# Optimization experiments

Hardware: AMD Instinct MI355X
Metric: run time of the kernel (lower is better)

Reference implementation:

```python
import jax, jax.numpy as jnp
import numpy as np

B, U, I, H = 1024, 8, 512, 512


def setup_inputs() -> dict:
    key = jax.random.key(0)
    ks = jax.random.split(key, 6)
    s_i = 1.0 / np.sqrt(H)  # torch GRU init: U(-1/sqrt(H), 1/sqrt(H))
    inputs = jax.random.normal(ks[0], (B, U, I), dtype=jnp.float32)
    hidden = jax.random.normal(ks[1], (B, U, H), dtype=jnp.float32)
    W_ih = jax.random.uniform(ks[2], (U, 3 * H, I), minval=-s_i, maxval=s_i, dtype=jnp.float32)
    W_hh = jax.random.uniform(ks[3], (U, 3 * H, H), minval=-s_i, maxval=s_i, dtype=jnp.float32)
    b_ih = jax.random.uniform(ks[4], (U, 3 * H), minval=-s_i, maxval=s_i, dtype=jnp.float32)
    b_hh = jax.random.uniform(ks[5], (U, 3 * H), minval=-s_i, maxval=s_i, dtype=jnp.float32)
    return {"inputs": inputs, "hidden": hidden, "W_ih": W_ih, "W_hh": W_hh, "b_ih": b_ih, "b_hh": b_hh}


def reference(inputs, hidden, W_ih, W_hh, b_ih, b_hh):
    # Grouped single-step GRU: all num_units cells computed in one batched matmul pair.
    # gx, gh: [B, U, 3H]
    gx = jnp.einsum('bui,ugi->bug', inputs, W_ih) + b_ih[None]
    gh = jnp.einsum('buh,ugh->bug', hidden, W_hh) + b_hh[None]
    xr, xz, xn = jnp.split(gx, 3, axis=-1)
    hr, hz, hn = jnp.split(gh, 3, axis=-1)
    r = jax.nn.sigmoid(xr + hr)
    z = jax.nn.sigmoid(xz + hz)
    n = jnp.tanh(xn + r * hn)
    return (1.0 - z) * n + z * hidden
```

## Files before the change

### kernel.cpp

```cpp
#include <hip/hip_runtime.h>
#include <hip/hip_bf16.h>
#include <stdint.h>


#define B_ 1024
#define U_ 8
#define I_ 512
#define H_ 512
#define KDIM 512

#define NX (B_ * U_ * I_)
#define NW (U_ * 3 * H_ * I_)
#define OFF_X 0
#define OFF_H NX
#define OFF_WIH (2 * NX)
#define OFF_WHH (2 * NX + NW)
#define NTOT (2 * NX + 2 * NW)
#define WS_NEED ((size_t)NTOT * 2)

#define BM 64
#define BN 64
#define BK 64
#define ESTR 68

typedef __attribute__((ext_vector_type(8))) short short8;
typedef __attribute__((ext_vector_type(4))) float floatx4;

__device__ __forceinline__ unsigned int pk2bf(float a, float b) {
    float2 f2; f2.x = a; f2.y = b;
    union { __hip_bfloat162 h; unsigned int u; } cv;
    cv.h = __float22bfloat162_rn(f2);
    return cv.u;
}

__device__ __forceinline__ void async16(const void* g, void* l) {
    __builtin_amdgcn_global_load_lds(
        (const __attribute__((address_space(1))) void*)g,
        (__attribute__((address_space(3))) void*)l, 16, 0, 0);
}

__global__ __launch_bounds__(256)
void convert_bf16_kernel(const float* __restrict__ x, const float* __restrict__ h,
                         const float* __restrict__ wih, const float* __restrict__ whh,
                         unsigned short* __restrict__ ws)
{
    const size_t base = ((size_t)blockIdx.x * 256 + threadIdx.x) * 8;
    const float* src; size_t off;
    if (base < (size_t)OFF_H)        { src = x;   off = OFF_X; }
    else if (base < (size_t)OFF_WIH) { src = h;   off = OFF_H; }
    else if (base < (size_t)OFF_WHH) { src = wih; off = OFF_WIH; }
    else                             { src = whh; off = OFF_WHH; }
    const float4 v0 = *(const float4*)(src + (base - off));
    const float4 v1 = *(const float4*)(src + (base - off) + 4);
    uint4 o;
    o.x = pk2bf(v0.x, v0.y);
    o.y = pk2bf(v0.z, v0.w);
    o.z = pk2bf(v1.x, v1.y);
    o.w = pk2bf(v1.z, v1.w);
    *(uint4*)(ws + base) = o;
}

union Smem {
    unsigned short bf[8][64 * 64];
    float ep[3][BM * ESTR];
};

__global__ __launch_bounds__(512, 4)
void gru_main_kernel(const unsigned short* __restrict__ ws,
                     const float* __restrict__ hidden,
                     const float* __restrict__ b_ih,
                     const float* __restrict__ b_hh,
                     float* __restrict__ out)
{
    const int u  = blockIdx.x >> 3;
    const int nb = blockIdx.x & 7;
    const int mb = blockIdx.y;
    const int b0 = mb * BM;
    const int h0 = nb * BN;

    const int tid  = threadIdx.x;
    const int lane = tid & 63;
    const int wave = tid >> 6;
    const int lr   = lane & 15;
    const int q    = lane >> 4;
    const int wm   = wave & 1;
    const int wn   = (wave >> 1) & 1;
    const int g2   = wave >> 2;

    __shared__ Smem smem;

    const unsigned short* gbase; int grstr;
    if (wave == 0)      { gbase = ws + OFF_X + ((size_t)b0 * U_ + u) * I_; grstr = U_ * I_; }
    else if (wave == 1) { gbase = ws + OFF_H + ((size_t)b0 * U_ + u) * H_; grstr = U_ * H_; }
    else if (wave <= 4) { int g = wave - 2; gbase = ws + OFF_WIH + ((size_t)(u * 3 + g) * H_ + h0) * I_; grstr = I_; }
    else                { int g = wave - 5; gbase = ws + OFF_WHH + ((size_t)(u * 3 + g) * H_ + h0) * H_; grstr = H_; }

    const int rsub = lane >> 3;
    const int lch  = (lane & 7) ^ rsub;

    floatx4 acc[3][2][2];
    #pragma unroll
    for (int g = 0; g < 3; ++g)
        #pragma unroll
        for (int mt = 0; mt < 2; ++mt)
            #pragma unroll
            for (int nt = 0; nt < 2; ++nt)
                acc[g][mt][nt] = (floatx4){0.f, 0.f, 0.f, 0.f};

    const int aslab = g2;
    const int bbase = 2 + 3 * g2;

    for (int k0 = 0; k0 < KDIM; k0 += BK) {
        #pragma unroll
        for (int i = 0; i < 8; ++i) {
            const int row = i * 8 + rsub;
            const unsigned short* g = gbase + (size_t)row * grstr + k0 + lch * 8;
            void* l = (void*)((char*)&smem.bf[wave][i * 512] + lane * 16);
            async16(g, l);
        }
        __syncthreads();

        short8 afr[2][2];
        #pragma unroll
        for (int mt = 0; mt < 2; ++mt)
            #pragma unroll
            for (int ks = 0; ks < 2; ++ks) {
                const int row = wm * 32 + mt * 16 + lr;
                const int ch  = (ks * 4 + q) ^ (lr & 7);
                afr[mt][ks] = *(const short8*)&smem.bf[aslab][row * 64 + ch * 8];
            }
        #pragma unroll
        for (int g = 0; g < 3; ++g)
            #pragma unroll
            for (int nt = 0; nt < 2; ++nt)
                #pragma unroll
                for (int ks = 0; ks < 2; ++ks) {
                    const int row = wn * 32 + nt * 16 + lr;
                    const int ch  = (ks * 4 + q) ^ (lr & 7);
                    const short8 bfr = *(const short8*)&smem.bf[bbase + g][row * 64 + ch * 8];
                    #pragma unroll
                    for (int mt = 0; mt < 2; ++mt)
                        acc[g][mt][nt] = __builtin_amdgcn_mfma_f32_16x16x32_bf16(
                            afr[mt][ks], bfr, acc[g][mt][nt], 0, 0, 0);
                }
        __syncthreads();
    }

    const float* bih = b_ih + u * (3 * H_);
    const float* bhh = b_hh + u * (3 * H_);

    if (g2 == 1) {
        #pragma unroll
        for (int nt = 0; nt < 2; ++nt) {
            const int col = wn * 32 + nt * 16 + lr;
            const float bhr = bhh[h0 + col];
            const float bhz = bhh[H_ + h0 + col];
            const float bhn = bhh[2 * H_ + h0 + col];
            #pragma unroll
            for (int mt = 0; mt < 2; ++mt)
                #pragma unroll
                for (int r = 0; r < 4; ++r) {
                    const int row = wm * 32 + mt * 16 + q * 4 + r;
                    smem.ep[0][row * ESTR + col] = acc[0][mt][nt][r] + bhr;
                    smem.ep[1][row * ESTR + col] = acc[1][mt][nt][r] + bhz;
                    smem.ep[2][row * ESTR + col] = acc[2][mt][nt][r] + bhn;
                }
        }
    }
    __syncthreads();

    if (g2 == 0) {
        #pragma unroll
        for (int nt = 0; nt < 2; ++nt) {
            const int col  = wn * 32 + nt * 16 + lr;
            const int hcol = h0 + col;
            const float bir  = bih[hcol];
            const float biz  = bih[H_ + hcol];
            const float bin_ = bih[2 * H_ + hcol];
            #pragma unroll
            for (int mt = 0; mt < 2; ++mt)
                #pragma unroll
                for (int r = 0; r < 4; ++r) {
                    const int row  = wm * 32 + mt * 16 + q * 4 + r;
                    const size_t gidx = ((size_t)(b0 + row) * U_ + u) * H_ + hcol;
                    const float hprev = hidden[gidx];
                    const float hr = smem.ep[0][row * ESTR + col];
                    const float hz = smem.ep[1][row * ESTR + col];
                    const float hn = smem.ep[2][row * ESTR + col];
                    const float xr = acc[0][mt][nt][r] + bir;
                    const float xz = acc[1][mt][nt][r] + biz;
                    const float xn = acc[2][mt][nt][r] + bin_;
                    const float rg = 1.f / (1.f + __expf(-(xr + hr)));
                    const float zg = 1.f / (1.f + __expf(-(xz + hz)));
                    const float ng = tanhf(xn + rg * hn);
                    out[gidx] = (1.f - zg) * ng + zg * hprev;
                }
        }
    }
}

#define LSTR 40
union SmemF {
    short bf[8][BM * LSTR];
    float ep[3][BM * ESTR];
};

__global__ __launch_bounds__(512, 4)
void gru_fallback_kernel(const float* __restrict__ inputs, const float* __restrict__ hidden,
                         const float* __restrict__ W_ih, const float* __restrict__ W_hh,
                         const float* __restrict__ b_ih, const float* __restrict__ b_hh,
                         float* __restrict__ out)
{
    const int nb = blockIdx.x;
    const int mb = blockIdx.y;
    const int u  = blockIdx.z;
    const int b0 = mb * BM, h0 = nb * BN;
    const int tid = threadIdx.x, lane = tid & 63, wave = tid >> 6;
    const int lr = lane & 15, q = lane >> 4;
    const int wm = wave & 1, wn = (wave >> 1) & 1, g2 = wave >> 2;

    __shared__ SmemF smem;

    const float* srcs[8]; int rstr[8];
    srcs[0] = inputs + ((size_t)b0 * U_ + u) * I_;         rstr[0] = U_ * I_;
    srcs[1] = hidden + ((size_t)b0 * U_ + u) * H_;         rstr[1] = U_ * H_;
    srcs[2] = W_ih + ((size_t)(u * 3 + 0) * H_ + h0) * I_; rstr[2] = I_;
    srcs[3] = W_ih + ((size_t)(u * 3 + 1) * H_ + h0) * I_; rstr[3] = I_;
    srcs[4] = W_ih + ((size_t)(u * 3 + 2) * H_ + h0) * I_; rstr[4] = I_;
    srcs[5] = W_hh + ((size_t)(u * 3 + 0) * H_ + h0) * H_; rstr[5] = H_;
    srcs[6] = W_hh + ((size_t)(u * 3 + 1) * H_ + h0) * H_; rstr[6] = H_;
    srcs[7] = W_hh + ((size_t)(u * 3 + 2) * H_ + h0) * H_; rstr[7] = H_;

    const int srow = tid >> 3, c4 = (tid & 7) * 4;
    const float* tb[8];
    #pragma unroll
    for (int s = 0; s < 8; ++s) tb[s] = srcs[s] + (size_t)srow * rstr[s] + c4;

    floatx4 acc[3][2][2];
    #pragma unroll
    for (int g = 0; g < 3; ++g)
        #pragma unroll
        for (int mt = 0; mt < 2; ++mt)
            #pragma unroll
            for (int nt = 0; nt < 2; ++nt) acc[g][mt][nt] = (floatx4){0.f, 0.f, 0.f, 0.f};

    const int aslab = g2, bbase = 2 + 3 * g2;
    float4 pre[8];
    #pragma unroll
    for (int s = 0; s < 8; ++s) pre[s] = *(const float4*)(tb[s]);

    for (int k0 = 0; k0 < KDIM; k0 += 32) {
        #pragma unroll
        for (int s = 0; s < 8; ++s) {
            uint2 w; w.x = pk2bf(pre[s].x, pre[s].y); w.y = pk2bf(pre[s].z, pre[s].w);
            *(uint2*)&smem.bf[s][srow * LSTR + c4] = w;
        }
        __syncthreads();
        if (k0 + 32 < KDIM) {
            #pragma unroll
            for (int s = 0; s < 8; ++s) pre[s] = *(const float4*)(tb[s] + k0 + 32);
        }
        short8 afr[2];
        #pragma unroll
        for (int mt = 0; mt < 2; ++mt)
            afr[mt] = *(const short8*)&smem.bf[aslab][(wm * 32 + mt * 16 + lr) * LSTR + q * 8];
        #pragma unroll
        for (int g = 0; g < 3; ++g) {
            const short8 bf0 = *(const short8*)&smem.bf[bbase + g][(wn * 32 + lr) * LSTR + q * 8];
            const short8 bf1 = *(const short8*)&smem.bf[bbase + g][(wn * 32 + 16 + lr) * LSTR + q * 8];
            #pragma unroll
            for (int mt = 0; mt < 2; ++mt) {
                acc[g][mt][0] = __builtin_amdgcn_mfma_f32_16x16x32_bf16(afr[mt], bf0, acc[g][mt][0], 0, 0, 0);
                acc[g][mt][1] = __builtin_amdgcn_mfma_f32_16x16x32_bf16(afr[mt], bf1, acc[g][mt][1], 0, 0, 0);
            }
        }
        __syncthreads();
    }

    const float* bih = b_ih + u * (3 * H_);
    const float* bhh = b_hh + u * (3 * H_);
    if (g2 == 1) {
        #pragma unroll
        for (int nt = 0; nt < 2; ++nt) {
            const int col = wn * 32 + nt * 16 + lr;
            const float bhr = bhh[h0 + col], bhz = bhh[H_ + h0 + col], bhn = bhh[2 * H_ + h0 + col];
            #pragma unroll
            for (int mt = 0; mt < 2; ++mt)
                #pragma unroll
                for (int r = 0; r < 4; ++r) {
                    const int row = wm * 32 + mt * 16 + q * 4 + r;
                    smem.ep[0][row * ESTR + col] = acc[0][mt][nt][r] + bhr;
                    smem.ep[1][row * ESTR + col] = acc[1][mt][nt][r] + bhz;
                    smem.ep[2][row * ESTR + col] = acc[2][mt][nt][r] + bhn;
                }
        }
    }
    __syncthreads();
    if (g2 == 0) {
        #pragma unroll
        for (int nt = 0; nt < 2; ++nt) {
            const int col = wn * 32 + nt * 16 + lr, hcol = h0 + col;
            const float bir = bih[hcol], biz = bih[H_ + hcol], bin_ = bih[2 * H_ + hcol];
            #pragma unroll
            for (int mt = 0; mt < 2; ++mt)
                #pragma unroll
                for (int r = 0; r < 4; ++r) {
                    const int row = wm * 32 + mt * 16 + q * 4 + r;
                    const size_t gidx = ((size_t)(b0 + row) * U_ + u) * H_ + hcol;
                    const float hprev = hidden[gidx];
                    const float hr = smem.ep[0][row * ESTR + col];
                    const float hz = smem.ep[1][row * ESTR + col];
                    const float hn = smem.ep[2][row * ESTR + col];
                    const float xr = acc[0][mt][nt][r] + bir;
                    const float xz = acc[1][mt][nt][r] + biz;
                    const float xn = acc[2][mt][nt][r] + bin_;
                    const float rg = 1.f / (1.f + __expf(-(xr + hr)));
                    const float zg = 1.f / (1.f + __expf(-(xz + hz)));
                    const float ng = tanhf(xn + rg * hn);
                    out[gidx] = (1.f - zg) * ng + zg * hprev;
                }
        }
    }
}

extern "C" void kernel_launch(void* const* d_in, const int* in_sizes, int n_in,
                              void* d_out, int out_size, void* d_ws, size_t ws_size,
                              hipStream_t stream) {
    const float* inputs = (const float*)d_in[0];
    const float* hidden = (const float*)d_in[1];
    const float* W_ih   = (const float*)d_in[2];
    const float* W_hh   = (const float*)d_in[3];
    const float* b_ih   = (const float*)d_in[4];
    const float* b_hh   = (const float*)d_in[5];
    float* out = (float*)d_out;

    if (ws_size >= WS_NEED) {
        unsigned short* ws = (unsigned short*)d_ws;
        convert_bf16_kernel<<<NTOT / 2048, 256, 0, stream>>>(inputs, hidden, W_ih, W_hh, ws);
        dim3 grid(64, 16, 1);
        gru_main_kernel<<<grid, 512, 0, stream>>>(ws, hidden, b_ih, b_hh, out);
    } else {
        dim3 grid(8, 16, 8);
        gru_fallback_kernel<<<grid, 512, 0, stream>>>(inputs, hidden, W_ih, W_hh, b_ih, b_hh, out);
    }
}
```

Before: 201.1 us.

## Double-buffer LDS tiles with BK=32 to overlap async loads and MFMA

Halves the K-tile to 32 and splits LDS into two buffers. The async global-to-LDS loads for the next tile are issued right after the barrier, so they overlap the MFMA work on the current tile, and each iteration now needs one barrier instead of two. The LDS layout is re-swizzled to pack two 32-wide rows per 128-byte line, with precomputed load and fragment offsets. Total LDS stays the same, but the loop runs twice as many iterations with less work each, which adds loop and barrier overhead.

```diff
diff --git a/kernel.cpp b/kernel.cpp
--- a/kernel.cpp
+++ b/kernel.cpp
@@ -20,7 +20,10 @@
 
 #define BM 64
 #define BN 64
-#define BK 64
+#define BK 32
+#define NITER (KDIM / BK)
+#define SLAB_B 4096
+#define BUF_B (8 * SLAB_B)
 #define ESTR 68
 
 typedef __attribute__((ext_vector_type(8))) short short8;
@@ -61,7 +64,7 @@
 }
 
 union Smem {
-    unsigned short bf[8][64 * 64];
+    char raw[2 * BUF_B];
     float ep[3][BM * ESTR];
 };
 
@@ -95,8 +98,34 @@
     else if (wave <= 4) { int g = wave - 2; gbase = ws + OFF_WIH + ((size_t)(u * 3 + g) * H_ + h0) * I_; grstr = I_; }
     else                { int g = wave - 5; gbase = ws + OFF_WHH + ((size_t)(u * 3 + g) * H_ + h0) * H_; grstr = H_; }
 
-    const int rsub = lane >> 3;
-    const int lch  = (lane & 7) ^ rsub;
+    const unsigned short* gptr[4];
+    int ldsoff[4];
+    #pragma unroll
+    for (int i = 0; i < 4; ++i) {
+        const int line = i * 8 + (lane >> 3);
+        const int pos  = (lane & 7) ^ (line & 7);
+        const int row  = 2 * line + (pos >> 2);
+        const int ch   = pos & 3;
+        gptr[i]   = gbase + (size_t)row * grstr + ch * 8;
+        ldsoff[i] = wave * SLAB_B + i * 1024 + lane * 16;
+    }
+
+    int aoff[2], boff[2];
+    #pragma unroll
+    for (int t = 0; t < 2; ++t) {
+        {
+            const int r = wm * 32 + t * 16 + lr;
+            const int line = r >> 1;
+            const int pp = (((r & 1) * 4 + q)) ^ (line & 7);
+            aoff[t] = line * 128 + pp * 16;
+        }
+        {
+            const int r = wn * 32 + t * 16 + lr;
+            const int line = r >> 1;
+            const int pp = (((r & 1) * 4 + q)) ^ (line & 7);
+            boff[t] = line * 128 + pp * 16;
+        }
+    }
 
     floatx4 acc[3][2][2];
     #pragma unroll
@@ -110,41 +139,40 @@
     const int aslab = g2;
     const int bbase = 2 + 3 * g2;
 
-    for (int k0 = 0; k0 < KDIM; k0 += BK) {
-        #pragma unroll
-        for (int i = 0; i < 8; ++i) {
-            const int row = i * 8 + rsub;
-            const unsigned short* g = gbase + (size_t)row * grstr + k0 + lch * 8;
-            void* l = (void*)((char*)&smem.bf[wave][i * 512] + lane * 16);
-            async16(g, l);
-        }
+    #pragma unroll
+    for (int i = 0; i < 4; ++i) {
+        async16(gptr[i], smem.raw + ldsoff[i]);
+        gptr[i] += BK;
+    }
+
+    for (int it = 0; it < NITER; ++it) {
+        const int cur = it & 1;
         __syncthreads();
 
-        short8 afr[2][2];
-        #pragma unroll
-        for (int mt = 0; mt < 2; ++mt)
-            #pragma unroll
-            for (int ks = 0; ks < 2; ++ks) {
-                const int row = wm * 32 + mt * 16 + lr;
-                const int ch  = (ks * 4 + q) ^ (lr & 7);
-                afr[mt][ks] = *(const short8*)&smem.bf[aslab][row * 64 + ch * 8];
+        if (it + 1 < NITER) {
+            const int nxtoff = ((it + 1) & 1) * BUF_B;
+            #pragma unroll
+            for (int i = 0; i < 4; ++i) {
+                async16(gptr[i], smem.raw + nxtoff + ldsoff[i]);
+                gptr[i] += BK;
             }
-        #pragma unroll
-        for (int g = 0; g < 3; ++g)
-            #pragma unroll
-            for (int nt = 0; nt < 2; ++nt)
-                #pragma unroll
-                for (int ks = 0; ks < 2; ++ks) {
-                    const int row = wn * 32 + nt * 16 + lr;
-                    const int ch  = (ks * 4 + q) ^ (lr & 7);
-                    const short8 bfr = *(const short8*)&smem.bf[bbase + g][row * 64 + ch * 8];
-                    #pragma unroll
-                    for (int mt = 0; mt < 2; ++mt)
-                        acc[g][mt][nt] = __builtin_amdgcn_mfma_f32_16x16x32_bf16(
-                            afr[mt][ks], bfr, acc[g][mt][nt], 0, 0, 0);
-                }
-        __syncthreads();
-    }
+        }
+
+        const char* base = smem.raw + cur * BUF_B;
+        const short8 a0 = *(const short8*)(base + aslab * SLAB_B + aoff[0]);
+        const short8 a1 = *(const short8*)(base + aslab * SLAB_B + aoff[1]);
+        #pragma unroll
+        for (int g = 0; g < 3; ++g) {
+            const char* bslab = base + (bbase + g) * SLAB_B;
+            #pragma unroll
+            for (int nt = 0; nt < 2; ++nt) {
+                const short8 bf = *(const short8*)(bslab + boff[nt]);
+                acc[g][0][nt] = __builtin_amdgcn_mfma_f32_16x16x32_bf16(a0, bf, acc[g][0][nt], 0, 0, 0);
+                acc[g][1][nt] = __builtin_amdgcn_mfma_f32_16x16x32_bf16(a1, bf, acc[g][1][nt], 0, 0, 0);
+            }
+        }
+    }
+    __syncthreads();
 
     const float* bih = b_ih + u * (3 * H_);
     const float* bhh = b_hh + u * (3 * H_);
```

Result: faster. 175.4 us (-12.8%).

## Replace LDS-tiled GRU GEMM with direct global-to-register MFMA fragments

Applied to the files above, without the earlier changes.

Rewrites the main GRU kernel so each wave loads bf16 MFMA operand fragments directly from global memory instead of staging 64x64 tiles in shared memory. Each wave computes a 16x32 tile for all six gates (input and hidden), which removes the LDS exchange and barriers in the epilogue. The grid is doubled with 256-thread blocks. This drops shared-memory staging and synchronization, but relies on L1/L2 caches for operand reuse and issues strided, less coalesced global loads.

```diff
diff --git a/kernel.cpp b/kernel.cpp
--- a/kernel.cpp
+++ b/kernel.cpp
@@ -18,11 +18,6 @@
 #define NTOT (2 * NX + 2 * NW)
 #define WS_NEED ((size_t)NTOT * 2)
 
-#define BM 64
-#define BN 64
-#define BK 64
-#define ESTR 68
-
 typedef __attribute__((ext_vector_type(8))) short short8;
 typedef __attribute__((ext_vector_type(4))) float floatx4;
 
@@ -31,12 +26,6 @@
     union { __hip_bfloat162 h; unsigned int u; } cv;
     cv.h = __float22bfloat162_rn(f2);
     return cv.u;
-}
-
-__device__ __forceinline__ void async16(const void* g, void* l) {
-    __builtin_amdgcn_global_load_lds(
-        (const __attribute__((address_space(1))) void*)g,
-        (__attribute__((address_space(3))) void*)l, 16, 0, 0);
 }
 
 __global__ __launch_bounds__(256)
@@ -60,149 +49,92 @@
     *(uint4*)(ws + base) = o;
 }
 
-union Smem {
-    unsigned short bf[8][64 * 64];
-    float ep[3][BM * ESTR];
-};
-
-__global__ __launch_bounds__(512, 4)
+__global__ __launch_bounds__(256, 4)
 void gru_main_kernel(const unsigned short* __restrict__ ws,
                      const float* __restrict__ hidden,
                      const float* __restrict__ b_ih,
                      const float* __restrict__ b_hh,
                      float* __restrict__ out)
 {
-    const int u  = blockIdx.x >> 3;
-    const int nb = blockIdx.x & 7;
-    const int mb = blockIdx.y;
-    const int b0 = mb * BM;
-    const int h0 = nb * BN;
-
-    const int tid  = threadIdx.x;
-    const int lane = tid & 63;
-    const int wave = tid >> 6;
-    const int lr   = lane & 15;
-    const int q    = lane >> 4;
-    const int wm   = wave & 1;
-    const int wn   = (wave >> 1) & 1;
-    const int g2   = wave >> 2;
-
-    __shared__ Smem smem;
-
-    const unsigned short* gbase; int grstr;
-    if (wave == 0)      { gbase = ws + OFF_X + ((size_t)b0 * U_ + u) * I_; grstr = U_ * I_; }
-    else if (wave == 1) { gbase = ws + OFF_H + ((size_t)b0 * U_ + u) * H_; grstr = U_ * H_; }
-    else if (wave <= 4) { int g = wave - 2; gbase = ws + OFF_WIH + ((size_t)(u * 3 + g) * H_ + h0) * I_; grstr = I_; }
-    else                { int g = wave - 5; gbase = ws + OFF_WHH + ((size_t)(u * 3 + g) * H_ + h0) * H_; grstr = H_; }
-
-    const int rsub = lane >> 3;
-    const int lch  = (lane & 7) ^ rsub;
-
-    floatx4 acc[3][2][2];
-    #pragma unroll
-    for (int g = 0; g < 3; ++g)
-        #pragma unroll
-        for (int mt = 0; mt < 2; ++mt)
-            #pragma unroll
-            for (int nt = 0; nt < 2; ++nt)
-                acc[g][mt][nt] = (floatx4){0.f, 0.f, 0.f, 0.f};
-
-    const int aslab = g2;
-    const int bbase = 2 + 3 * g2;
-
-    for (int k0 = 0; k0 < KDIM; k0 += BK) {
-        #pragma unroll
-        for (int i = 0; i < 8; ++i) {
-            const int row = i * 8 + rsub;
-            const unsigned short* g = gbase + (size_t)row * grstr + k0 + lch * 8;
-            void* l = (void*)((char*)&smem.bf[wave][i * 512] + lane * 16);
-            async16(g, l);
-        }
-        __syncthreads();
-
-        short8 afr[2][2];
-        #pragma unroll
-        for (int mt = 0; mt < 2; ++mt)
-            #pragma unroll
-            for (int ks = 0; ks < 2; ++ks) {
-                const int row = wm * 32 + mt * 16 + lr;
-                const int ch  = (ks * 4 + q) ^ (lr & 7);
-                afr[mt][ks] = *(const short8*)&smem.bf[aslab][row * 64 + ch * 8];
+    const int un  = blockIdx.x;
+    const int u   = un >> 4;
+    const int n0  = (un & 15) * 32;
+    const int lane = threadIdx.x & 63;
+    const int wave = threadIdx.x >> 6;
+    const int m0  = (blockIdx.y * 4 + wave) * 16;
+    const int lr  = lane & 15;
+    const int q   = lane >> 4;
+
+    const unsigned short* xp = ws + OFF_X + ((size_t)(m0 + lr) * U_ + u) * I_ + q * 8;
+    const unsigned short* hp = ws + OFF_H + ((size_t)(m0 + lr) * U_ + u) * H_ + q * 8;
+
+    const unsigned short* wbase[6];
+    #pragma unroll
+    for (int g = 0; g < 3; ++g) {
+        wbase[g]     = ws + OFF_WIH + (size_t)(u * 3 + g) * (H_ * I_);
+        wbase[g + 3] = ws + OFF_WHH + (size_t)(u * 3 + g) * (H_ * I_);
+    }
+    int voff[2];
+    #pragma unroll
+    for (int nt = 0; nt < 2; ++nt)
+        voff[nt] = (n0 + nt * 16 + lr) * I_ + q * 8;
+
+    floatx4 acc[6][2];
+    #pragma unroll
+    for (int g = 0; g < 6; ++g)
+        #pragma unroll
+        for (int nt = 0; nt < 2; ++nt)
+            acc[g][nt] = (floatx4){0.f, 0.f, 0.f, 0.f};
+
+    #pragma unroll
+    for (int it = 0; it < KDIM / 32; ++it) {
+        const int k0 = it * 32;
+        const short8 ax = *(const short8*)(xp + k0);
+        const short8 ah = *(const short8*)(hp + k0);
+        #pragma unroll
+        for (int g = 0; g < 3; ++g) {
+            #pragma unroll
+            for (int nt = 0; nt < 2; ++nt) {
+                const short8 bx = *(const short8*)(wbase[g] + voff[nt] + k0);
+                const short8 bh = *(const short8*)(wbase[g + 3] + voff[nt] + k0);
+                acc[g][nt]     = __builtin_amdgcn_mfma_f32_16x16x32_bf16(ax, bx, acc[g][nt], 0, 0, 0);
+                acc[g + 3][nt] = __builtin_amdgcn_mfma_f32_16x16x32_bf16(ah, bh, acc[g + 3][nt], 0, 0, 0);
             }
-        #pragma unroll
-        for (int g = 0; g < 3; ++g)
-            #pragma unroll
-            for (int nt = 0; nt < 2; ++nt)
-                #pragma unroll
-                for (int ks = 0; ks < 2; ++ks) {
-                    const int row = wn * 32 + nt * 16 + lr;
-                    const int ch  = (ks * 4 + q) ^ (lr & 7);
-                    const short8 bfr = *(const short8*)&smem.bf[bbase + g][row * 64 + ch * 8];
-                    #pragma unroll
-                    for (int mt = 0; mt < 2; ++mt)
-                        acc[g][mt][nt] = __builtin_amdgcn_mfma_f32_16x16x32_bf16(
-                            afr[mt][ks], bfr, acc[g][mt][nt], 0, 0, 0);
-                }
-        __syncthreads();
+        }
     }
 
     const float* bih = b_ih + u * (3 * H_);
     const float* bhh = b_hh + u * (3 * H_);
-
-    if (g2 == 1) {
-        #pragma unroll
-        for (int nt = 0; nt < 2; ++nt) {
-            const int col = wn * 32 + nt * 16 + lr;
-            const float bhr = bhh[h0 + col];
-            const float bhz = bhh[H_ + h0 + col];
-            const float bhn = bhh[2 * H_ + h0 + col];
-            #pragma unroll
-            for (int mt = 0; mt < 2; ++mt)
-                #pragma unroll
-                for (int r = 0; r < 4; ++r) {
-                    const int row = wm * 32 + mt * 16 + q * 4 + r;
-                    smem.ep[0][row * ESTR + col] = acc[0][mt][nt][r] + bhr;
-                    smem.ep[1][row * ESTR + col] = acc[1][mt][nt][r] + bhz;
-                    smem.ep[2][row * ESTR + col] = acc[2][mt][nt][r] + bhn;
-                }
-        }
-    }
-    __syncthreads();
-
-    if (g2 == 0) {
-        #pragma unroll
-        for (int nt = 0; nt < 2; ++nt) {
-            const int col  = wn * 32 + nt * 16 + lr;
-            const int hcol = h0 + col;
-            const float bir  = bih[hcol];
-            const float biz  = bih[H_ + hcol];
-            const float bin_ = bih[2 * H_ + hcol];
-            #pragma unroll
-            for (int mt = 0; mt < 2; ++mt)
-                #pragma unroll
-                for (int r = 0; r < 4; ++r) {
-                    const int row  = wm * 32 + mt * 16 + q * 4 + r;
-                    const size_t gidx = ((size_t)(b0 + row) * U_ + u) * H_ + hcol;
-                    const float hprev = hidden[gidx];
-                    const float hr = smem.ep[0][row * ESTR + col];
-                    const float hz = smem.ep[1][row * ESTR + col];
-                    const float hn = smem.ep[2][row * ESTR + col];
-                    const float xr = acc[0][mt][nt][r] + bir;
-                    const float xz = acc[1][mt][nt][r] + biz;
-                    const float xn = acc[2][mt][nt][r] + bin_;
-                    const float rg = 1.f / (1.f + __expf(-(xr + hr)));
-                    const float zg = 1.f / (1.f + __expf(-(xz + hz)));
-                    const float ng = tanhf(xn + rg * hn);
-                    out[gidx] = (1.f - zg) * ng + zg * hprev;
-                }
+    #pragma unroll
+    for (int nt = 0; nt < 2; ++nt) {
+        const int col = n0 + nt * 16 + lr;
+        const float bir  = bih[col],          bhr = bhh[col];
+        const float biz  = bih[H_ + col],     bhz = bhh[H_ + col];
+        const float bin_ = bih[2 * H_ + col], bhn = bhh[2 * H_ + col];
+        #pragma unroll
+        for (int r = 0; r < 4; ++r) {
+            const int row = m0 + q * 4 + r;
+            const size_t gidx = ((size_t)row * U_ + u) * H_ + col;
+            const float hprev = hidden[gidx];
+            const float xr = acc[0][nt][r] + bir;
+            const float xz = acc[1][nt][r] + biz;
+            const float xn = acc[2][nt][r] + bin_;
+            const float hr = acc[3][nt][r] + bhr;
+            const float hz = acc[4][nt][r] + bhz;
+            const float hn = acc[5][nt][r] + bhn;
+            const float rg = 1.f / (1.f + __expf(-(xr + hr)));
+            const float zg = 1.f / (1.f + __expf(-(xz + hz)));
+            const float ng = tanhf(xn + rg * hn);
+            out[gidx] = (1.f - zg) * ng + zg * hprev;
         }
     }
 }
 
 #define LSTR 40
+#define ESTR 68
 union SmemF {
-    short bf[8][BM * LSTR];
-    float ep[3][BM * ESTR];
+    short bf[8][64 * LSTR];
+    float ep[3][64 * ESTR];
 };
 
 __global__ __launch_bounds__(512, 4)
@@ -214,7 +146,7 @@
     const int nb = blockIdx.x;
     const int mb = blockIdx.y;
     const int u  = blockIdx.z;
-    const int b0 = mb * BM, h0 = nb * BN;
+    const int b0 = mb * 64, h0 = nb * 64;
     const int tid = threadIdx.x, lane = tid & 63, wave = tid >> 6;
     const int lr = lane & 15, q = lane >> 4;
     const int wm = wave & 1, wn = (wave >> 1) & 1, g2 = wave >> 2;
@@ -337,8 +269,8 @@
     if (ws_size >= WS_NEED) {
         unsigned short* ws = (unsigned short*)d_ws;
         convert_bf16_kernel<<<NTOT / 2048, 256, 0, stream>>>(inputs, hidden, W_ih, W_hh, ws);
-        dim3 grid(64, 16, 1);
-        gru_main_kernel<<<grid, 512, 0, stream>>>(ws, hidden, b_ih, b_hh, out);
+        dim3 grid(128, 16, 1);
+        gru_main_kernel<<<grid, 256, 0, stream>>>(ws, hidden, b_ih, b_hh, out);
     } else {
         dim3 grid(8, 16, 8);
         gru_fallback_kernel<<<grid, 512, 0, stream>>>(inputs, hidden, W_ih, W_hh, b_ih, b_hh, out);
```

Result: slower. 324.5 us (+61.4%).
